# Kernel optimization log

Hardware: AMD Instinct MI355X
Metric: run time of the kernel (lower is better)

Reference implementation:

```python
import jax, jax.numpy as jnp
import numpy as np

N = 8192   # nodes
D = 128    # uniform feature dim (arch = [128,128,128])
L = 2      # num_layers = len(arch)-1
EDGE_P = 0.01

def setup_inputs() -> dict:
    key = jax.random.key(0)
    ks = jax.random.split(key, 11)
    features = jax.random.normal(ks[0], (N, D), dtype=jnp.float32)
    # sparse symmetric adjacency with self-loops (diagonal forced True, as in forward)
    a = jax.random.uniform(ks[1], (N, N)) < EDGE_P
    mask = a | a.T | jnp.eye(N, dtype=bool)
    s = 1.0 / np.sqrt(D)
    def w(k):
        return (jax.random.normal(k, (L, D, D), dtype=jnp.float32) * s)
    def b(k):
        return jax.random.normal(k, (L, D), dtype=jnp.float32) * 0.01
    return {
        "features": features, "mask": mask,
        "Wq": w(ks[2]), "bq": b(ks[3]),
        "Wk": w(ks[4]), "bk": b(ks[5]),
        "Wv": w(ks[6]), "bv": b(ks[7]),
        "Wo": w(ks[8]), "bo": b(ks[9]),
    }

def reference(features, mask, Wq, bq, Wk, bk, Wv, bv, Wo, bo):
    h = features
    outputs = [h]
    for l in range(L):
        Q = h @ Wq[l] + bq[l]                      # [N, D]
        K = h @ Wk[l] + bk[l]
        V = h @ Wv[l] + bv[l]
        scores = (Q @ K.T) * (1.0 / jnp.sqrt(jnp.float32(K.shape[1])))  # [N, N]
        scores = jnp.where(mask, scores, -jnp.inf)
        attn = jax.nn.softmax(scores, axis=1)
        h = attn @ V                                # [N, D]
        h = h @ Wo[l] + bo[l]
        outputs.append(h)
    return tuple(outputs)
```

## Files before the change

kernel.cpp:

```cpp
#include <hip/hip_runtime.h>
#include <hip/hip_bf16.h>
#include <hip/hip_fp16.h>
#include <math.h>

#define N 8192
#define D 128
#define CAP 512

typedef _Float16 f16x2 __attribute__((ext_vector_type(2)));
typedef _Float16 f16x4 __attribute__((ext_vector_type(4)));
typedef _Float16 f16x8 __attribute__((ext_vector_type(8)));

__device__ __forceinline__ float dot2(f16x2 a, f16x2 b, float c) {
#if __has_builtin(__builtin_amdgcn_fdot2)
    return __builtin_amdgcn_fdot2(a, b, c, false);
#else
    return c + (float)a[0] * (float)b[0] + (float)a[1] * (float)b[1];
#endif
}

__device__ __forceinline__ float dot8(f16x8 a, f16x8 b, float c) {
    c = dot2(__builtin_shufflevector(a, a, 0, 1), __builtin_shufflevector(b, b, 0, 1), c);
    c = dot2(__builtin_shufflevector(a, a, 2, 3), __builtin_shufflevector(b, b, 2, 3), c);
    c = dot2(__builtin_shufflevector(a, a, 4, 5), __builtin_shufflevector(b, b, 4, 5), c);
    c = dot2(__builtin_shufflevector(a, a, 6, 7), __builtin_shufflevector(b, b, 6, 7), c);
    return c;
}

__global__ __launch_bounds__(256) void build_adj(const int* __restrict__ mask,
                                                 unsigned short* __restrict__ nbr,
                                                 int* __restrict__ deg) {
    const int i = blockIdx.x;
    __shared__ int cnt;
    if (threadIdx.x == 0) cnt = 0;
    __syncthreads();
    const int4* row = (const int4*)(mask + (size_t)i * N);
    for (int c = threadIdx.x; c < N / 4; c += 256) {
        int4 m4 = row[c];
        int base = 4 * c;
        if (m4.x) { int p = atomicAdd(&cnt, 1); if (p < CAP) nbr[(size_t)i * CAP + p] = (unsigned short)(base); }
        if (m4.y) { int p = atomicAdd(&cnt, 1); if (p < CAP) nbr[(size_t)i * CAP + p] = (unsigned short)(base + 1); }
        if (m4.z) { int p = atomicAdd(&cnt, 1); if (p < CAP) nbr[(size_t)i * CAP + p] = (unsigned short)(base + 2); }
        if (m4.w) { int p = atomicAdd(&cnt, 1); if (p < CAP) nbr[(size_t)i * CAP + p] = (unsigned short)(base + 3); }
    }
    __syncthreads();
    if (threadIdx.x == 0) deg[i] = (cnt > CAP) ? CAP : cnt;
}

__global__ __launch_bounds__(256) void qkv_gemm(const float* __restrict__ A,
                                                const float* __restrict__ Wq, const float* __restrict__ bq,
                                                const float* __restrict__ Wk, const float* __restrict__ bk,
                                                const float* __restrict__ Wv, const float* __restrict__ bv,
                                                __half* __restrict__ Qo, __half* __restrict__ Ko,
                                                __half* __restrict__ Vo,
                                                float* __restrict__ copy_out) {
    __shared__ float As[8][D];
    const int tid = threadIdx.x;
    const int r   = tid >> 5;
    const int jg  = tid & 31;
    const int i0  = blockIdx.x * 8;

    const float4 av = ((const float4*)(A + (size_t)i0 * D))[tid];
    ((float4*)&As[0][0])[tid] = av;
    ((float4*)(copy_out + (size_t)i0 * D))[tid] = av;
    __syncthreads();

    const float* Ws[3] = {Wq, Wk, Wv};
    const float* bs[3] = {bq, bk, bv};
    __half* Os[3] = {Qo, Ko, Vo};

    #pragma unroll
    for (int m = 0; m < 3; ++m) {
        float4 acc = *(const float4*)(bs[m] + 4 * jg);
        const float* W = Ws[m];
        #pragma unroll 8
        for (int k4 = 0; k4 < 32; ++k4) {
            const float4 a4 = *(const float4*)&As[r][4 * k4];
            const float* wb = W + (size_t)(4 * k4) * D + 4 * jg;
            const float4 w0 = *(const float4*)(wb);
            const float4 w1 = *(const float4*)(wb + D);
            const float4 w2 = *(const float4*)(wb + 2 * D);
            const float4 w3 = *(const float4*)(wb + 3 * D);
            acc.x += a4.x * w0.x + a4.y * w1.x + a4.z * w2.x + a4.w * w3.x;
            acc.y += a4.x * w0.y + a4.y * w1.y + a4.z * w2.y + a4.w * w3.y;
            acc.z += a4.x * w0.z + a4.y * w1.z + a4.z * w2.z + a4.w * w3.z;
            acc.w += a4.x * w0.w + a4.y * w1.w + a4.z * w2.w + a4.w * w3.w;
        }
        f16x4 h;
        h[0] = (_Float16)acc.x; h[1] = (_Float16)acc.y;
        h[2] = (_Float16)acc.z; h[3] = (_Float16)acc.w;
        *(f16x4*)(Os[m] + (size_t)(i0 + r) * D + 4 * jg) = h;
    }
}

__global__ __launch_bounds__(256) void gemmO_qkv(const float* __restrict__ Aattn,
                                                 const float* __restrict__ Wo, const float* __restrict__ bo,
                                                 float* __restrict__ Hout,
                                                 const float* __restrict__ Wq, const float* __restrict__ bq,
                                                 const float* __restrict__ Wk, const float* __restrict__ bk,
                                                 const float* __restrict__ Wv, const float* __restrict__ bv,
                                                 __half* __restrict__ Qo, __half* __restrict__ Ko,
                                                 __half* __restrict__ Vo) {
    __shared__ float As[8][D];
    __shared__ float Hs[8][D];
    const int tid = threadIdx.x;
    const int r   = tid >> 5;
    const int jg  = tid & 31;
    const int i0  = blockIdx.x * 8;

    ((float4*)&As[0][0])[tid] = ((const float4*)(Aattn + (size_t)i0 * D))[tid];
    __syncthreads();

    {
        float4 acc = *(const float4*)(bo + 4 * jg);
        #pragma unroll 8
        for (int k4 = 0; k4 < 32; ++k4) {
            const float4 a4 = *(const float4*)&As[r][4 * k4];
            const float* wb = Wo + (size_t)(4 * k4) * D + 4 * jg;
            const float4 w0 = *(const float4*)(wb);
            const float4 w1 = *(const float4*)(wb + D);
            const float4 w2 = *(const float4*)(wb + 2 * D);
            const float4 w3 = *(const float4*)(wb + 3 * D);
            acc.x += a4.x * w0.x + a4.y * w1.x + a4.z * w2.x + a4.w * w3.x;
            acc.y += a4.x * w0.y + a4.y * w1.y + a4.z * w2.y + a4.w * w3.y;
            acc.z += a4.x * w0.z + a4.y * w1.z + a4.z * w2.z + a4.w * w3.z;
            acc.w += a4.x * w0.w + a4.y * w1.w + a4.z * w2.w + a4.w * w3.w;
        }
        *(float4*)(Hout + (size_t)(i0 + r) * D + 4 * jg) = acc;
        *(float4*)&Hs[r][4 * jg] = acc;
    }
    __syncthreads();

    const float* Ws[3] = {Wq, Wk, Wv};
    const float* bs[3] = {bq, bk, bv};
    __half* Os[3] = {Qo, Ko, Vo};
    #pragma unroll
    for (int m = 0; m < 3; ++m) {
        float4 acc = *(const float4*)(bs[m] + 4 * jg);
        const float* W = Ws[m];
        #pragma unroll 8
        for (int k4 = 0; k4 < 32; ++k4) {
            const float4 a4 = *(const float4*)&Hs[r][4 * k4];
            const float* wb = W + (size_t)(4 * k4) * D + 4 * jg;
            const float4 w0 = *(const float4*)(wb);
            const float4 w1 = *(const float4*)(wb + D);
            const float4 w2 = *(const float4*)(wb + 2 * D);
            const float4 w3 = *(const float4*)(wb + 3 * D);
            acc.x += a4.x * w0.x + a4.y * w1.x + a4.z * w2.x + a4.w * w3.x;
            acc.y += a4.x * w0.y + a4.y * w1.y + a4.z * w2.y + a4.w * w3.y;
            acc.z += a4.x * w0.z + a4.y * w1.z + a4.z * w2.z + a4.w * w3.z;
            acc.w += a4.x * w0.w + a4.y * w1.w + a4.z * w2.w + a4.w * w3.w;
        }
        f16x4 h;
        h[0] = (_Float16)acc.x; h[1] = (_Float16)acc.y;
        h[2] = (_Float16)acc.z; h[3] = (_Float16)acc.w;
        *(f16x4*)(Os[m] + (size_t)(i0 + r) * D + 4 * jg) = h;
    }
}

__global__ __launch_bounds__(256) void gemm_bias(const float* __restrict__ A,
                                                 const float* __restrict__ W,
                                                 const float* __restrict__ bias,
                                                 float* __restrict__ C) {
    __shared__ float As[8][D];
    const int tid = threadIdx.x;
    const int r   = tid >> 5;
    const int jg  = tid & 31;
    const int i0  = blockIdx.x * 8;

    ((float4*)&As[0][0])[tid] = ((const float4*)(A + (size_t)i0 * D))[tid];
    __syncthreads();

    float4 acc = *(const float4*)(bias + 4 * jg);
    #pragma unroll 8
    for (int k4 = 0; k4 < 32; ++k4) {
        const float4 a4 = *(const float4*)&As[r][4 * k4];
        const float* wb = W + (size_t)(4 * k4) * D + 4 * jg;
        const float4 w0 = *(const float4*)(wb);
        const float4 w1 = *(const float4*)(wb + D);
        const float4 w2 = *(const float4*)(wb + 2 * D);
        const float4 w3 = *(const float4*)(wb + 3 * D);
        acc.x += a4.x * w0.x + a4.y * w1.x + a4.z * w2.x + a4.w * w3.x;
        acc.y += a4.x * w0.y + a4.y * w1.y + a4.z * w2.y + a4.w * w3.y;
        acc.z += a4.x * w0.z + a4.y * w1.z + a4.z * w2.z + a4.w * w3.z;
        acc.w += a4.x * w0.w + a4.y * w1.w + a4.z * w2.w + a4.w * w3.w;
    }
    *(float4*)(C + (size_t)(i0 + r) * D + 4 * jg) = acc;
}

__global__ __launch_bounds__(256) void attn_sparse(const __half* __restrict__ Q,
                                                   const __half* __restrict__ K,
                                                   const __half* __restrict__ V,
                                                   const unsigned short* __restrict__ nbr,
                                                   const int* __restrict__ deg,
                                                   float* __restrict__ Hout) {
    const int tid  = threadIdx.x;
    const int wave = tid >> 6;
    const int lane = tid & 63;
    const int g    = lane >> 4;
    const int gl   = lane & 15;
    const int i    = blockIdx.x * 4 + wave;

    __shared__ unsigned short jls[4][CAP];

    const int dg = min(deg[i], CAP);
    for (int e = lane; e < dg; e += 64)
        jls[wave][e] = nbr[(size_t)i * CAP + e];
    const f16x8 qv = ((const f16x8*)(Q + (size_t)i * D))[gl];
    __syncthreads();

    const float scale = 0.088388347648318447f;

    float acc[8] = {0.f, 0.f, 0.f, 0.f, 0.f, 0.f, 0.f, 0.f};
    float denom  = 0.f;

    for (int e = g; e < dg; e += 4) {
        const int j = jls[wave][e];
        const f16x8 kv = ((const f16x8*)(K + (size_t)j * D))[gl];
        float dot = dot8(kv, qv, 0.f);
        dot += __shfl_xor(dot, 1);
        dot += __shfl_xor(dot, 2);
        dot += __shfl_xor(dot, 4);
        dot += __shfl_xor(dot, 8);
        const float p = __expf(dot * scale);
        const f16x8 v8 = ((const f16x8*)(V + (size_t)j * D))[gl];
        #pragma unroll
        for (int k = 0; k < 8; ++k) acc[k] += p * (float)v8[k];
        denom += p;
    }

    #pragma unroll
    for (int k = 0; k < 8; ++k) {
        acc[k] += __shfl_xor(acc[k], 16);
        acc[k] += __shfl_xor(acc[k], 32);
    }
    denom += __shfl_xor(denom, 16);
    denom += __shfl_xor(denom, 32);

    if (g == 0) {
        const float inv = 1.0f / denom;
        float4 o0, o1;
        o0.x = acc[0] * inv; o0.y = acc[1] * inv; o0.z = acc[2] * inv; o0.w = acc[3] * inv;
        o1.x = acc[4] * inv; o1.y = acc[5] * inv; o1.z = acc[6] * inv; o1.w = acc[7] * inv;
        float4* dst = (float4*)(Hout + (size_t)i * D + 8 * gl);
        dst[0] = o0;
        dst[1] = o1;
    }
}

extern "C" void kernel_launch(void* const* d_in, const int* in_sizes, int n_in,
                              void* d_out, int out_size, void* d_ws, size_t ws_size,
                              hipStream_t stream) {
    const float* features = (const float*)d_in[0];
    const int*   mask     = (const int*)d_in[1];
    const float* Wq = (const float*)d_in[2];
    const float* bq = (const float*)d_in[3];
    const float* Wk = (const float*)d_in[4];
    const float* bk = (const float*)d_in[5];
    const float* Wv = (const float*)d_in[6];
    const float* bv = (const float*)d_in[7];
    const float* Wo = (const float*)d_in[8];
    const float* bo = (const float*)d_in[9];
    float* out = (float*)d_out;

    char* base = (char*)d_ws;
    unsigned short* nbr = (unsigned short*)base;
    int*    deg  = (int*)(base + (size_t)N * CAP * 2);
    __half* Qb16 = (__half*)(base + (size_t)N * CAP * 2 + N * 4);
    __half* Kb16 = Qb16 + (size_t)N * D;
    __half* Vb16 = Kb16 + (size_t)N * D;
    float*  tmp  = (float*)(Vb16 + (size_t)N * D);

    build_adj<<<N, 256, 0, stream>>>(mask, nbr, deg);

    qkv_gemm<<<N / 8, 256, 0, stream>>>(features, Wq, bq, Wk, bk, Wv, bv,
                                        Qb16, Kb16, Vb16, out);
    attn_sparse<<<N / 4, 256, 0, stream>>>(Qb16, Kb16, Vb16, nbr, deg, tmp);
    gemmO_qkv<<<N / 8, 256, 0, stream>>>(tmp, Wo, bo, out + (size_t)N * D,
                                         Wq + D * D, bq + D, Wk + D * D, bk + D,
                                         Wv + D * D, bv + D, Qb16, Kb16, Vb16);
    attn_sparse<<<N / 4, 256, 0, stream>>>(Qb16, Kb16, Vb16, nbr, deg, tmp);
    gemm_bias<<<N / 8, 256, 0, stream>>>(tmp, Wo + D * D, bo + D,
                                         out + (size_t)2 * N * D);
}
```

Baseline: 577.1 us.

## Interleave K and V rows and process neighbors in node-range phases

K and V are now stored interleaved in one buffer with row stride 2*D, so each neighbor's key and value sit in one contiguous 512-byte row and their loads issue together. The attention loop also runs four passes over the neighbor list, each handling only neighbors whose index falls in one quarter of the node range. The aim is for concurrent waves to touch a smaller KV working set at a time and get more L2 reuse. The cost is scanning the neighbor list four times, with divergent skips inside each pass.

After: 615.8 us. +6.7%, slower.

```diff
diff --git a/kernel.cpp b/kernel.cpp
--- a/kernel.cpp
+++ b/kernel.cpp
@@ -68,6 +68,7 @@
     const float* Ws[3] = {Wq, Wk, Wv};
     const float* bs[3] = {bq, bk, bv};
     __half* Os[3] = {Qo, Ko, Vo};
+    const size_t st[3] = {D, 2 * D, 2 * D};
 
     #pragma unroll
     for (int m = 0; m < 3; ++m) {
@@ -89,7 +90,7 @@
         f16x4 h;
         h[0] = (_Float16)acc.x; h[1] = (_Float16)acc.y;
         h[2] = (_Float16)acc.z; h[3] = (_Float16)acc.w;
-        *(f16x4*)(Os[m] + (size_t)(i0 + r) * D + 4 * jg) = h;
+        *(f16x4*)(Os[m] + (size_t)(i0 + r) * st[m] + 4 * jg) = h;
     }
 }
 
@@ -134,6 +135,7 @@
     const float* Ws[3] = {Wq, Wk, Wv};
     const float* bs[3] = {bq, bk, bv};
     __half* Os[3] = {Qo, Ko, Vo};
+    const size_t st[3] = {D, 2 * D, 2 * D};
     #pragma unroll
     for (int m = 0; m < 3; ++m) {
         float4 acc = *(const float4*)(bs[m] + 4 * jg);
@@ -154,7 +156,7 @@
         f16x4 h;
         h[0] = (_Float16)acc.x; h[1] = (_Float16)acc.y;
         h[2] = (_Float16)acc.z; h[3] = (_Float16)acc.w;
-        *(f16x4*)(Os[m] + (size_t)(i0 + r) * D + 4 * jg) = h;
+        *(f16x4*)(Os[m] + (size_t)(i0 + r) * st[m] + 4 * jg) = h;
     }
 }
 
@@ -189,8 +191,7 @@
 }
 
 __global__ __launch_bounds__(256) void attn_sparse(const __half* __restrict__ Q,
-                                                   const __half* __restrict__ K,
-                                                   const __half* __restrict__ V,
+                                                   const __half* __restrict__ KV,
                                                    const unsigned short* __restrict__ nbr,
                                                    const int* __restrict__ deg,
                                                    float* __restrict__ Hout) {
@@ -214,19 +215,24 @@
     float acc[8] = {0.f, 0.f, 0.f, 0.f, 0.f, 0.f, 0.f, 0.f};
     float denom  = 0.f;
 
-    for (int e = g; e < dg; e += 4) {
-        const int j = jls[wave][e];
-        const f16x8 kv = ((const f16x8*)(K + (size_t)j * D))[gl];
-        float dot = dot8(kv, qv, 0.f);
-        dot += __shfl_xor(dot, 1);
-        dot += __shfl_xor(dot, 2);
-        dot += __shfl_xor(dot, 4);
-        dot += __shfl_xor(dot, 8);
-        const float p = __expf(dot * scale);
-        const f16x8 v8 = ((const f16x8*)(V + (size_t)j * D))[gl];
-        #pragma unroll
-        for (int k = 0; k < 8; ++k) acc[k] += p * (float)v8[k];
-        denom += p;
+    #pragma unroll 1
+    for (int ph = 0; ph < 4; ++ph) {
+        for (int e = g; e < dg; e += 4) {
+            const int j = jls[wave][e];
+            if ((j >> 11) != ph) continue;
+            const f16x8* kvp = (const f16x8*)(KV + (size_t)j * (2 * D));
+            const f16x8 kv = kvp[gl];
+            const f16x8 v8 = kvp[16 + gl];
+            float dot = dot8(kv, qv, 0.f);
+            dot += __shfl_xor(dot, 1);
+            dot += __shfl_xor(dot, 2);
+            dot += __shfl_xor(dot, 4);
+            dot += __shfl_xor(dot, 8);
+            const float p = __expf(dot * scale);
+            #pragma unroll
+            for (int k = 0; k < 8; ++k) acc[k] += p * (float)v8[k];
+            denom += p;
+        }
     }
 
     #pragma unroll
@@ -267,19 +273,18 @@
     unsigned short* nbr = (unsigned short*)base;
     int*    deg  = (int*)(base + (size_t)N * CAP * 2);
     __half* Qb16 = (__half*)(base + (size_t)N * CAP * 2 + N * 4);
-    __half* Kb16 = Qb16 + (size_t)N * D;
-    __half* Vb16 = Kb16 + (size_t)N * D;
-    float*  tmp  = (float*)(Vb16 + (size_t)N * D);
+    __half* KVb  = Qb16 + (size_t)N * D;
+    float*  tmp  = (float*)(KVb + (size_t)N * 2 * D);
 
     build_adj<<<N, 256, 0, stream>>>(mask, nbr, deg);
 
     qkv_gemm<<<N / 8, 256, 0, stream>>>(features, Wq, bq, Wk, bk, Wv, bv,
-                                        Qb16, Kb16, Vb16, out);
-    attn_sparse<<<N / 4, 256, 0, stream>>>(Qb16, Kb16, Vb16, nbr, deg, tmp);
+                                        Qb16, KVb, KVb + D, out);
+    attn_sparse<<<N / 4, 256, 0, stream>>>(Qb16, KVb, nbr, deg, tmp);
     gemmO_qkv<<<N / 8, 256, 0, stream>>>(tmp, Wo, bo, out + (size_t)N * D,
                                          Wq + D * D, bq + D, Wk + D * D, bk + D,
-                                         Wv + D * D, bv + D, Qb16, Kb16, Vb16);
-    attn_sparse<<<N / 4, 256, 0, stream>>>(Qb16, Kb16, Vb16, nbr, deg, tmp);
+                                         Wv + D * D, bv + D, Qb16, KVb, KVb + D);
+    attn_sparse<<<N / 4, 256, 0, stream>>>(Qb16, KVb, nbr, deg, tmp);
     gemm_bias<<<N / 8, 256, 0, stream>>>(tmp, Wo + D * D, bo + D,
                                          out + (size_t)2 * N * D);
 }
```
